# Kernel tuning notes

Measured on AMD Instinct MI355X. Metric: run time of the kernel, lower is better.

The kernel has to match this reference:

```python
import jax, jax.numpy as jnp
import numpy as np

EPS = 1e-6
DIAG_SIZE = 128  # triu band half-width (init kwarg diag_size)
NEG_INF = -1e9


def feature_map(x):
    # tanh feature map: phi(x) = tanh(x) + 1 (positive feature map)
    return jnp.tanh(x) + 1.0


def causal_dot_product(Q, K, V):
    # Q,K: [N,L,H,E], V: [N,L,H,D]
    # running KV state: S_l = sum_{s<=l} K_s V_s^T, materialized via cumsum
    kv = jnp.cumsum(jnp.einsum('nlhe,nlhd->nlhed', K, V), axis=1)  # [N,L,H,E,D]
    return jnp.einsum('nlhe,nlhed->nlhd', Q, kv)


def setup_inputs() -> dict:
    key = jax.random.key(0)
    k1, k2, k3 = jax.random.split(key, 3)
    N, L, H, E = 2, 2048, 8, 64
    queries = jax.random.normal(k1, (N, L, H, E), dtype=jnp.float32)
    keys = jax.random.normal(k2, (N, L, H, E), dtype=jnp.float32)
    values = jax.random.normal(k3, (N, L, H, E), dtype=jnp.float32)
    key_lengths_mask = jnp.ones((N, L), dtype=jnp.float32)  # all keys valid
    blend = jnp.full((1,), 0.9, dtype=jnp.float32)  # learned blend param (init 0.9)
    return {"queries": queries, "keys": keys, "values": values,
            "key_lengths_mask": key_lengths_mask, "blend": blend}


def reference(queries, keys, values, key_lengths_mask, blend):
    N, L, H, E = queries.shape
    # ---- linear attention path (kernel_1 = tanh, kernel_2 = 'none') ----
    Q1 = feature_map(queries)
    K1 = feature_map(keys) * key_lengths_mask[:, :, None, None]
    Z1 = 1.0 / (jnp.einsum('nlhi,nlhi->nlh', Q1, jnp.cumsum(K1, axis=1)) + EPS)
    LV = causal_dot_product(Q1, K1, values) * Z1[..., None]  # [N,L,H,D]
    # ---- full softmax attention path (banded by triu) ----
    softmax_temp = 1.0 / np.sqrt(E).astype(np.float32)
    QK = jnp.einsum('nlhe,nshe->nhls', queries, keys)  # [N,H,L,L]
    l_idx = jnp.arange(L)[:, None]
    s_idx = jnp.arange(L)[None, :]
    causal_add = jnp.where(s_idx <= l_idx, 0.0, NEG_INF)  # lower-triangular mask
    key_add = jnp.where(key_lengths_mask > 0, 0.0, NEG_INF)  # [N,L]
    logits = softmax_temp * (QK + causal_add[None, None] + key_add[:, None, None, :])
    A = jax.nn.softmax(logits, axis=-1)
    # torch.triu(A, diagonal=-diag_size): keep s >= l - diag_size
    band = s_idx >= (l_idx - DIAG_SIZE)
    A = jnp.where(band[None, None], A, 0.0)
    # dropout: eval mode (identity)
    SV = jnp.einsum('nhls,nshd->nlhd', A, values)
    b = blend[0]
    return b * SV + (1.0 - b) * LV
```

## Files before the change

kernel.cpp:

```cpp
#include <hip/hip_runtime.h>
#include <math.h>

#define N_ 2
#define L_ 2048
#define H_ 8
#define E_ 64
#define D_ 64
#define C_ 128
#define NC (L_/C_)
#define ROWSTRIDE (H_*E_)
#define TEMP 0.125f
#define EPS_F 1e-6f
#define NEG_INF_F (-1e9f)
#define CHUNK_WS (E_*D_ + E_)
#define NCHUNKS (N_*H_*NC)
#define TPAD 136
#define PPAD 72

typedef __attribute__((ext_vector_type(8))) short short8;
typedef __attribute__((ext_vector_type(4))) float f32x4;

__device__ __forceinline__ short f2bf(float x) {
  unsigned u = __float_as_uint(x);
  u += 0x7fffu + ((u >> 16) & 1u);
  return (short)(u >> 16);
}
__device__ __forceinline__ float bf2f(short s) {
  return __uint_as_float(((unsigned)(unsigned short)s) << 16);
}
__device__ __forceinline__ float tanh1f(float x) {
  float e = __expf(-2.f * x);
  return 2.f * __builtin_amdgcn_rcpf(1.f + e);
}

__device__ __forceinline__ void load_bf16_tile(short* __restrict__ dst,
                                               const float* __restrict__ src) {
  const int t = threadIdx.x;
#pragma unroll
  for (int it = 0; it < 4; ++it) {
    int gi = it * 256 + t;
    int row = gi >> 3, g = gi & 7;
    const float* p = src + row * ROWSTRIDE + g * 8;
    float4 a = *(const float4*)p;
    float4 b = *(const float4*)(p + 4);
    short8 v;
    v[0] = f2bf(a.x); v[1] = f2bf(a.y); v[2] = f2bf(a.z); v[3] = f2bf(a.w);
    v[4] = f2bf(b.x); v[5] = f2bf(b.y); v[6] = f2bf(b.z); v[7] = f2bf(b.w);
    int sg = g ^ (row & 7);
    *(short8*)(dst + row * 64 + sg * 8) = v;
  }
}

__device__ __forceinline__ short8 frag_ld(const short* __restrict__ buf,
                                          int rowbase, int hf, int lane) {
  int r = rowbase + (lane & 15);
  int g = (hf * 4 + (lane >> 4)) ^ (r & 7);
  return *(const short8*)(buf + r * 64 + g * 8);
}
__device__ __forceinline__ short8 frag_ldT(const short* __restrict__ buf,
                                           int nbase, int g, int lane) {
  int r = nbase + (lane & 15);
  return *(const short8*)(buf + r * TPAD + g * 8);
}
__device__ __forceinline__ short8 frag_ldP(const short* __restrict__ buf,
                                           int rowbase, int ks, int lane) {
  int r = rowbase + (lane & 15);
  int g = ks * 4 + (lane >> 4);
  return *(const short8*)(buf + r * PPAD + g * 8);
}

extern "C" __global__ void __launch_bounds__(256, 4)
k_pre(const float* __restrict__ Q, const float* __restrict__ K,
      const float* __restrict__ V, const float* __restrict__ mask,
      float* __restrict__ ws, float* __restrict__ part) {
  __shared__ short ldsA[64 * TPAD];
  __shared__ short ldsB[64 * TPAD];
  __shared__ float fmsk[C_];
  const int orig = blockIdx.x;
  const int swz = (orig & 7) * 304 + (orig >> 3);
  const int t = threadIdx.x;
  const int w = t >> 6, lane = t & 63;
  const int col_lo = lane & 15;

  if (swz < 2176) {
    const int nh = swz / 136;
    const int p = swz - nh * 136;
    int qb = (int)((sqrtf(8.f * p + 1.f) - 1.f) * 0.5f);
    while ((qb + 1) * (qb + 2) / 2 <= p) ++qb;
    while (qb * (qb + 1) / 2 > p) --qb;
    const int kb = p - qb * (qb + 1) / 2;
    const int h = nh & (H_ - 1), n = nh >> 3;

    load_bf16_tile(ldsA, Q + ((n * L_ + qb * C_) * H_ + h) * E_);
    load_bf16_tile(ldsB, K + ((n * L_ + kb * C_) * H_ + h) * E_);
    if (t < C_) fmsk[t] = mask[n * L_ + kb * C_ + t];
    __syncthreads();

    const int rowbase = w * 32;
    short8 afr[2][2];
#pragma unroll
    for (int m = 0; m < 2; ++m)
#pragma unroll
      for (int hh = 0; hh < 2; ++hh)
        afr[m][hh] = frag_ld(ldsA, rowbase + 16 * m, hh, lane);

    f32x4 acc[2][8];
#pragma unroll
    for (int m = 0; m < 2; ++m)
#pragma unroll
      for (int c = 0; c < 8; ++c) acc[m][c] = (f32x4){0.f, 0.f, 0.f, 0.f};

#pragma unroll
    for (int c = 0; c < 8; ++c) {
      short8 b0 = frag_ld(ldsB, 16 * c, 0, lane);
      short8 b1 = frag_ld(ldsB, 16 * c, 1, lane);
#pragma unroll
      for (int m = 0; m < 2; ++m) {
        acc[m][c] = __builtin_amdgcn_mfma_f32_16x16x32_bf16(afr[m][0], b0, acc[m][c], 0, 0, 0);
        acc[m][c] = __builtin_amdgcn_mfma_f32_16x16x32_bf16(afr[m][1], b1, acc[m][c], 0, 0, 0);
      }
    }

    const bool diag = (kb == qb);
    float* pout = part + (size_t)(nh * NC + qb) * C_ * 16;
#pragma unroll
    for (int m = 0; m < 2; ++m) {
      const int rbase = rowbase + 16 * m + (lane >> 4) * 4;
      float rs[4] = {0.f, 0.f, 0.f, 0.f};
#pragma unroll
      for (int c = 0; c < 8; ++c) {
        const int col = 16 * c + col_lo;
        const float madd = (fmsk[col] > 0.f) ? 0.f : NEG_INF_F;
#pragma unroll
        for (int reg = 0; reg < 4; ++reg) {
          float x = acc[m][c][reg] + madd;
          if (diag && col > rbase + reg) x += NEG_INF_F;
          rs[reg] += __expf(x * TEMP);
        }
      }
#pragma unroll
      for (int off = 1; off < 16; off <<= 1) {
#pragma unroll
        for (int reg = 0; reg < 4; ++reg) rs[reg] += __shfl_xor(rs[reg], off);
      }
      if (col_lo == 0) {
#pragma unroll
        for (int reg = 0; reg < 4; ++reg) pout[(rbase + reg) * 16 + kb] = rs[reg];
      }
    }
  } else {
    const int id = swz - 2176;
    const int nh = id >> 4, c = id & 15;
    const int h = nh & (H_ - 1), n = nh >> 3;
    const int gbase = ((n * L_ + c * C_) * H_ + h) * E_;
    const int e = t & 63, sb = t >> 6;
    const int mbase = n * L_ + c * C_;
#pragma unroll
    for (int q = 0; q < 4; ++q) {
      int s0 = sb * 32 + q * 8;
      short8 kk, vv;
#pragma unroll
      for (int j = 0; j < 8; ++j) {
        float kx = K[gbase + (s0 + j) * ROWSTRIDE + e];
        kk[j] = f2bf(tanh1f(kx) * mask[mbase + s0 + j]);
        vv[j] = f2bf(V[gbase + (s0 + j) * ROWSTRIDE + e]);
      }
      *(short8*)(ldsA + e * TPAD + (s0 >> 3) * 8) = kk;
      *(short8*)(ldsB + e * TPAD + (s0 >> 3) * 8) = vv;
    }
    __syncthreads();

    f32x4 acc[4];
#pragma unroll
    for (int nn = 0; nn < 4; ++nn) acc[nn] = (f32x4){0.f, 0.f, 0.f, 0.f};
#pragma unroll
    for (int ks = 0; ks < 4; ++ks) {
      short8 a = frag_ldT(ldsB, 16 * w, ks * 4 + (lane >> 4), lane);
#pragma unroll
      for (int nn = 0; nn < 4; ++nn) {
        short8 b = frag_ldT(ldsA, 16 * nn, ks * 4 + (lane >> 4), lane);
        acc[nn] = __builtin_amdgcn_mfma_f32_16x16x32_bf16(a, b, acc[nn], 0, 0, 0);
      }
    }
    float* wsc = ws + (size_t)(nh * NC + c) * CHUNK_WS;
    const int drow = 16 * w + ((lane >> 4) << 2);
#pragma unroll
    for (int nn = 0; nn < 4; ++nn)
#pragma unroll
      for (int reg = 0; reg < 4; ++reg)
        wsc[(16 * nn + col_lo) * D_ + drow + reg] = acc[nn][reg];
    if (t < 64) {
      float s = 0.f;
#pragma unroll
      for (int g = 0; g < 16; ++g) {
        short8 v = *(const short8*)(ldsA + t * TPAD + g * 8);
#pragma unroll
        for (int j = 0; j < 8; ++j) s += bf2f(v[j]);
      }
      wsc[E_ * D_ + t] = s;
    }
  }
}

extern "C" __global__ void __launch_bounds__(256)
k_scan(float* __restrict__ ws) {
  const int bid = blockIdx.x;
  const int swz = (bid & 7) * 34 + (bid >> 3);
  const int nh = swz / 17, seg = swz - nh * 17;
  const int idx = seg * 256 + threadIdx.x;
  if (idx >= CHUNK_WS) return;
  float* base = ws + (size_t)nh * NC * CHUNK_WS + idx;
  float v[NC];
#pragma unroll
  for (int c = 0; c < NC; ++c) v[c] = base[(size_t)c * CHUNK_WS];
  float acc = 0.f;
#pragma unroll
  for (int c = 0; c < NC; ++c) {
    base[(size_t)c * CHUNK_WS] = acc;
    acc += v[c];
  }
}

extern "C" __global__ void __launch_bounds__(256, 3)
k_fused(const float* __restrict__ Q, const float* __restrict__ K,
        const float* __restrict__ V, const float* __restrict__ mask,
        const float* __restrict__ blend, const float* __restrict__ ws,
        const float* __restrict__ part, float* __restrict__ out) {
  __shared__ short kbuf[C_ * 64];
  __shared__ short kv[64 * TPAD];
  __shared__ short pbuf[64 * PPAD];
  __shared__ float zlds[64];
  __shared__ float dinv[64];
  __shared__ float ksum[E_];
  __shared__ float kmskC[C_];
  __shared__ float kmskP[C_];

  const int orig = blockIdx.x;
  const int swz = (orig & 7) * 64 + (orig >> 3);
  const int rh = swz & 1, qb = (swz >> 1) & (NC - 1), nh = swz >> 5;
  const int h = nh & (H_ - 1), n = nh >> 3;
  const int t = threadIdx.x;
  const int w = t >> 6, lane = t & 63;
  const int rowbase = w * 16;
  const int col_lo = lane & 15;
  const int rb = rowbase + ((lane >> 4) << 2);
  const int rtile0 = rh * 64 + rb;
  const int qgbase = ((n * L_ + qb * C_ + rh * 64) * H_ + h) * E_;
  const int kbase_chunk = ((n * L_ + qb * C_) * H_ + h) * E_;
  const float* wsc = ws + (size_t)(nh * NC + qb) * CHUNK_WS;
  const float bl = blend[0];
  const float ob = 1.f - bl;
  const int d = t & 63, sb = t >> 6;
  const bool haveprev = (qb > 0);
  const int kgp = ((n * L_ + (qb - 1) * C_) * H_ + h) * E_;

  float4 qraw[2][2];
  {
    const float* qp = Q + qgbase + (rowbase + (lane & 15)) * ROWSTRIDE;
#pragma unroll
    for (int kh = 0; kh < 2; ++kh) {
      int c0 = (kh * 4 + (lane >> 4)) * 8;
      qraw[kh][0] = *(const float4*)(qp + c0);
      qraw[kh][1] = *(const float4*)(qp + c0 + 4);
    }
  }
  short8 kraw[4];
  {
    const float* mrow = mask + n * L_ + qb * C_;
#pragma unroll
    for (int it = 0; it < 4; ++it) {
      int gi = it * 256 + t, row = gi >> 3, g = gi & 7;
      const float* p = K + kbase_chunk + row * ROWSTRIDE + g * 8;
      float4 a = *(const float4*)p, b = *(const float4*)(p + 4);
      float km = mrow[row];
      float xs[8] = {a.x, a.y, a.z, a.w, b.x, b.y, b.z, b.w};
      short8 vr, v1;
#pragma unroll
      for (int j = 0; j < 8; ++j) { vr[j] = f2bf(xs[j]); v1[j] = f2bf(tanh1f(xs[j]) * km); }
      kraw[it] = vr;
      *(short8*)(kbuf + row * 64 + (g ^ (row & 7)) * 8) = v1;
    }
  }
  {
    int eb = t >> 6;
#pragma unroll
    for (int q = 0; q < 2; ++q) {
      int e0 = eb * 16 + q * 8;
      short8 v;
#pragma unroll
      for (int j = 0; j < 8; ++j) v[j] = f2bf(wsc[(e0 + j) * D_ + d]);
      *(short8*)(kv + d * TPAD + (e0 >> 3) * 8) = v;
    }
  }
  short8 vcur[4];
#pragma unroll
  for (int q = 0; q < 4; ++q) {
#pragma unroll
    for (int j = 0; j < 8; ++j)
      vcur[q][j] = f2bf(V[kbase_chunk + (sb * 32 + q * 8 + j) * ROWSTRIDE + d]);
  }
  if (t < 64) {
    ksum[t] = wsc[E_ * D_ + t];
    const float* pb = part + ((size_t)(nh * NC + qb) * C_ + rh * 64 + t) * 16;
    float4 a = *(const float4*)pb, b = *(const float4*)(pb + 4);
    float4 c = *(const float4*)(pb + 8), d4 = *(const float4*)(pb + 12);
    float vv[16] = {a.x, a.y, a.z, a.w, b.x, b.y, b.z, b.w,
                    c.x, c.y, c.z, c.w, d4.x, d4.y, d4.z, d4.w};
    float s = 0.f;
#pragma unroll
    for (int j = 0; j < 16; ++j) s += (j <= qb) ? vv[j] : 0.f;
    dinv[t] = 1.f / s;
  }
  if (t < C_) {
    kmskC[t] = mask[n * L_ + qb * C_ + t];
    kmskP[t] = haveprev ? mask[n * L_ + (qb - 1) * C_ + t] : 1.f;
  }
  __syncthreads();

  short8 af1[2], afs[2];
#pragma unroll
  for (int kh = 0; kh < 2; ++kh) {
    float xs[8] = {qraw[kh][0].x, qraw[kh][0].y, qraw[kh][0].z, qraw[kh][0].w,
                   qraw[kh][1].x, qraw[kh][1].y, qraw[kh][1].z, qraw[kh][1].w};
#pragma unroll
    for (int j = 0; j < 8; ++j) { afs[kh][j] = f2bf(xs[j]); af1[kh][j] = f2bf(tanh1f(xs[j])); }
  }
  f32x4 c1[8];
#pragma unroll
  for (int ct = 0; ct < 8; ++ct) c1[ct] = (f32x4){0.f, 0.f, 0.f, 0.f};
#pragma unroll
  for (int ct = 0; ct < 8; ++ct) {
    short8 b0 = frag_ld(kbuf, 16 * ct, 0, lane);
    short8 b1 = frag_ld(kbuf, 16 * ct, 1, lane);
    c1[ct] = __builtin_amdgcn_mfma_f32_16x16x32_bf16(af1[0], b0, c1[ct], 0, 0, 0);
    c1[ct] = __builtin_amdgcn_mfma_f32_16x16x32_bf16(af1[1], b1, c1[ct], 0, 0, 0);
  }
  {
    float zz = 0.f;
#pragma unroll
    for (int kh = 0; kh < 2; ++kh) {
      int cb = (kh * 4 + (lane >> 4)) * 8;
#pragma unroll
      for (int j = 0; j < 8; ++j) zz += bf2f(af1[kh][j]) * ksum[cb + j];
    }
    zz += __shfl_xor(zz, 16);
    zz += __shfl_xor(zz, 32);
    if (lane < 16) zlds[rowbase + lane] = zz;
  }
  float rs[4] = {0.f, 0.f, 0.f, 0.f};
#pragma unroll
  for (int ct = 0; ct < 8; ++ct) {
    int col = 16 * ct + col_lo;
#pragma unroll
    for (int reg = 0; reg < 4; ++reg) {
      if (col <= rtile0 + reg) rs[reg] += c1[ct][reg];
      else c1[ct][reg] = 0.f;
    }
  }
#pragma unroll
  for (int off = 1; off < 16; off <<= 1)
#pragma unroll
    for (int reg = 0; reg < 4; ++reg) rs[reg] += __shfl_xor(rs[reg], off);

  f32x4 accL[4];
#pragma unroll
  for (int nn = 0; nn < 4; ++nn) accL[nn] = (f32x4){0.f, 0.f, 0.f, 0.f};
#pragma unroll
  for (int ks = 0; ks < 2; ++ks) {
    short8 bf[4];
#pragma unroll
    for (int nn = 0; nn < 4; ++nn)
      bf[nn] = frag_ldT(kv, 16 * nn, ks * 4 + (lane >> 4), lane);
#pragma unroll
    for (int nn = 0; nn < 4; ++nn)
      accL[nn] = __builtin_amdgcn_mfma_f32_16x16x32_bf16(af1[ks], bf[nn], accL[nn], 0, 0, 0);
  }
  __syncthreads();

#pragma unroll
  for (int it = 0; it < 4; ++it) {
    int gi = it * 256 + t, row = gi >> 3, g = gi & 7;
    *(short8*)(kbuf + row * 64 + (g ^ (row & 7)) * 8) = kraw[it];
  }
#pragma unroll
  for (int q = 0; q < 4; ++q)
    *(short8*)(kv + d * TPAD + ((sb * 32 + q * 8) >> 3) * 8) = vcur[q];
  __syncthreads();

  short8 pk[4], pv[4];
  if (haveprev) {
#pragma unroll
    for (int it = 0; it < 4; ++it) {
      int gi = it * 256 + t, row = gi >> 3, g = gi & 7;
      const float* p = K + kgp + row * ROWSTRIDE + g * 8;
      float4 a = *(const float4*)p, b = *(const float4*)(p + 4);
      float xs[8] = {a.x, a.y, a.z, a.w, b.x, b.y, b.z, b.w};
#pragma unroll
      for (int j = 0; j < 8; ++j) pk[it][j] = f2bf(xs[j]);
    }
#pragma unroll
    for (int q = 0; q < 4; ++q)
#pragma unroll
      for (int j = 0; j < 8; ++j)
        pv[q][j] = f2bf(V[kgp + (sb * 32 + q * 8 + j) * ROWSTRIDE + d]);
  }
#pragma unroll
  for (int hh = 0; hh < 2; ++hh) {
#pragma unroll
    for (int ch = 0; ch < 4; ++ch) {
      int ct = 4 * hh + ch, colh = 16 * ch + col_lo;
#pragma unroll
      for (int reg = 0; reg < 4; ++reg)
        pbuf[(rb + reg) * PPAD + colh] = f2bf(c1[ct][reg]);
    }
#pragma unroll
    for (int ks = 0; ks < 2; ++ks) {
      short8 ap = frag_ldP(pbuf, rowbase, ks, lane);
      short8 bv[4];
#pragma unroll
      for (int nn = 0; nn < 4; ++nn)
        bv[nn] = frag_ldT(kv, 16 * nn, 8 * hh + ks * 4 + (lane >> 4), lane);
#pragma unroll
      for (int nn = 0; nn < 4; ++nn)
        accL[nn] = __builtin_amdgcn_mfma_f32_16x16x32_bf16(ap, bv[nn], accL[nn], 0, 0, 0);
    }
  }
  f32x4 accS[4];
#pragma unroll
  for (int nn = 0; nn < 4; ++nn) accS[nn] = (f32x4){0.f, 0.f, 0.f, 0.f};
  {
    f32x4 cs[8];
#pragma unroll
    for (int ct = 0; ct < 8; ++ct) cs[ct] = (f32x4){0.f, 0.f, 0.f, 0.f};
#pragma unroll
    for (int ct = 0; ct < 8; ++ct) {
      short8 b0 = frag_ld(kbuf, 16 * ct, 0, lane);
      short8 b1 = frag_ld(kbuf, 16 * ct, 1, lane);
      cs[ct] = __builtin_amdgcn_mfma_f32_16x16x32_bf16(afs[0], b0, cs[ct], 0, 0, 0);
      cs[ct] = __builtin_amdgcn_mfma_f32_16x16x32_bf16(afs[1], b1, cs[ct], 0, 0, 0);
    }
#pragma unroll
    for (int ct = 0; ct < 8; ++ct) {
      int col = 16 * ct + col_lo;
      float madd = (kmskC[col] > 0.f) ? 0.f : NEG_INF_F;
#pragma unroll
      for (int reg = 0; reg < 4; ++reg) {
        float x = cs[ct][reg] + madd;
        if (col > rtile0 + reg) x += NEG_INF_F;
        cs[ct][reg] = __expf(x * TEMP);
      }
    }
#pragma unroll
    for (int hh = 0; hh < 2; ++hh) {
#pragma unroll
      for (int ch = 0; ch < 4; ++ch) {
        int ct = 4 * hh + ch, colh = 16 * ch + col_lo;
#pragma unroll
        for (int reg = 0; reg < 4; ++reg)
          pbuf[(rb + reg) * PPAD + colh] = f2bf(cs[ct][reg]);
      }
#pragma unroll
      for (int ks = 0; ks < 2; ++ks) {
        short8 ap = frag_ldP(pbuf, rowbase, ks, lane);
        short8 bv[4];
#pragma unroll
        for (int nn = 0; nn < 4; ++nn)
          bv[nn] = frag_ldT(kv, 16 * nn, 8 * hh + ks * 4 + (lane >> 4), lane);
#pragma unroll
        for (int nn = 0; nn < 4; ++nn)
          accS[nn] = __builtin_amdgcn_mfma_f32_16x16x32_bf16(ap, bv[nn], accS[nn], 0, 0, 0);
      }
    }
  }

  if (haveprev) {
    __syncthreads();
#pragma unroll
    for (int it = 0; it < 4; ++it) {
      int gi = it * 256 + t, row = gi >> 3, g = gi & 7;
      *(short8*)(kbuf + row * 64 + (g ^ (row & 7)) * 8) = pk[it];
    }
#pragma unroll
    for (int q = 0; q < 4; ++q)
      *(short8*)(kv + d * TPAD + ((sb * 32 + q * 8) >> 3) * 8) = pv[q];
    __syncthreads();

    f32x4 cs[8];
#pragma unroll
    for (int ct = 0; ct < 8; ++ct) cs[ct] = (f32x4){0.f, 0.f, 0.f, 0.f};
#pragma unroll
    for (int ct = 0; ct < 8; ++ct) {
      short8 b0 = frag_ld(kbuf, 16 * ct, 0, lane);
      short8 b1 = frag_ld(kbuf, 16 * ct, 1, lane);
      cs[ct] = __builtin_amdgcn_mfma_f32_16x16x32_bf16(afs[0], b0, cs[ct], 0, 0, 0);
      cs[ct] = __builtin_amdgcn_mfma_f32_16x16x32_bf16(afs[1], b1, cs[ct], 0, 0, 0);
    }
#pragma unroll
    for (int ct = 0; ct < 8; ++ct) {
      int col = 16 * ct + col_lo;
      float madd = (kmskP[col] > 0.f) ? 0.f : NEG_INF_F;
#pragma unroll
      for (int reg = 0; reg < 4; ++reg) {
        float x = cs[ct][reg] + madd;
        float pp = __expf(x * TEMP);
        if (col < rtile0 + reg) pp = 0.f;
        cs[ct][reg] = pp;
      }
    }
#pragma unroll
    for (int hh = 0; hh < 2; ++hh) {
#pragma unroll
      for (int ch = 0; ch < 4; ++ch) {
        int ct = 4 * hh + ch, colh = 16 * ch + col_lo;
#pragma unroll
        for (int reg = 0; reg < 4; ++reg)
          pbuf[(rb + reg) * PPAD + colh] = f2bf(cs[ct][reg]);
      }
#pragma unroll
      for (int ks = 0; ks < 2; ++ks) {
        short8 ap = frag_ldP(pbuf, rowbase, ks, lane);
        short8 bv[4];
#pragma unroll
        for (int nn = 0; nn < 4; ++nn)
          bv[nn] = frag_ldT(kv, 16 * nn, 8 * hh + ks * 4 + (lane >> 4), lane);
#pragma unroll
        for (int nn = 0; nn < 4; ++nn)
          accS[nn] = __builtin_amdgcn_mfma_f32_16x16x32_bf16(ap, bv[nn], accS[nn], 0, 0, 0);
      }
    }
  }

  float zrf[4], sdv[4];
#pragma unroll
  for (int reg = 0; reg < 4; ++reg) {
    zrf[reg] = ob / (zlds[rb + reg] + rs[reg] + EPS_F);
    sdv[reg] = bl * dinv[rb + reg];
  }
#pragma unroll
  for (int nn = 0; nn < 4; ++nn)
#pragma unroll
    for (int reg = 0; reg < 4; ++reg)
      out[qgbase + (rb + reg) * ROWSTRIDE + 16 * nn + col_lo] =
          zrf[reg] * accL[nn][reg] + sdv[reg] * accS[nn][reg];
}

extern "C" void kernel_launch(void* const* d_in, const int* in_sizes, int n_in,
                              void* d_out, int out_size, void* d_ws, size_t ws_size,
                              hipStream_t stream) {
  (void)in_sizes; (void)n_in; (void)out_size; (void)ws_size;
  const float* Q = (const float*)d_in[0];
  const float* K = (const float*)d_in[1];
  const float* V = (const float*)d_in[2];
  const float* mask = (const float*)d_in[3];
  const float* blend = (const float*)d_in[4];
  float* out = (float*)d_out;
  float* ws = (float*)d_ws;
  float* part = ws + (size_t)NCHUNKS * CHUNK_WS;

  k_pre<<<dim3(2432), dim3(256), 0, stream>>>(Q, K, V, mask, ws, part);
  k_scan<<<dim3(272), dim3(256), 0, stream>>>(ws);
  k_fused<<<dim3(N_ * H_ * NC * 2), dim3(256), 0, stream>>>(Q, K, V, mask, blend, ws, part, out);
}
```

Measured before the change: 52.86 us.

## Move banded softmax P·V and intra-chunk linear attention into the pre-pass kernel

New measurement: 55.90 us. +5.7%, slower.

```diff
diff --git a/kernel.cpp b/kernel.cpp
--- a/kernel.cpp
+++ b/kernel.cpp
@@ -33,8 +33,9 @@
   return 2.f * __builtin_amdgcn_rcpf(1.f + e);
 }
 
-__device__ __forceinline__ void load_bf16_tile(short* __restrict__ dst,
-                                               const float* __restrict__ src) {
+template <typename F>
+__device__ __forceinline__ void stage_tile(short* __restrict__ dst,
+                                           const float* __restrict__ src, F f) {
   const int t = threadIdx.x;
 #pragma unroll
   for (int it = 0; it < 4; ++it) {
@@ -43,11 +44,25 @@
     const float* p = src + row * ROWSTRIDE + g * 8;
     float4 a = *(const float4*)p;
     float4 b = *(const float4*)(p + 4);
+    float xs[8] = {a.x, a.y, a.z, a.w, b.x, b.y, b.z, b.w};
     short8 v;
-    v[0] = f2bf(a.x); v[1] = f2bf(a.y); v[2] = f2bf(a.z); v[3] = f2bf(a.w);
-    v[4] = f2bf(b.x); v[5] = f2bf(b.y); v[6] = f2bf(b.z); v[7] = f2bf(b.w);
-    int sg = g ^ (row & 7);
-    *(short8*)(dst + row * 64 + sg * 8) = v;
+#pragma unroll
+    for (int j = 0; j < 8; ++j) v[j] = f2bf(f(xs[j], row));
+    *(short8*)(dst + row * 64 + (g ^ (row & 7)) * 8) = v;
+  }
+}
+
+__device__ __forceinline__ void stage_vT(short* __restrict__ vt,
+                                         const float* __restrict__ Vbase) {
+  const int t = threadIdx.x;
+  const int d = t & 63, sb = t >> 6;
+#pragma unroll
+  for (int q = 0; q < 4; ++q) {
+    int s0 = sb * 32 + q * 8;
+    short8 v;
+#pragma unroll
+    for (int j = 0; j < 8; ++j) v[j] = f2bf(Vbase[(s0 + j) * ROWSTRIDE + d]);
+    *(short8*)(vt + d * TPAD + (s0 >> 3) * 8) = v;
   }
 }
 
@@ -69,15 +84,69 @@
   return *(const short8*)(buf + r * PPAD + g * 8);
 }
 
-extern "C" __global__ void __launch_bounds__(256, 4)
+__device__ __forceinline__ void pv_and_store(f32x4 acc[2][8], short* __restrict__ vt,
+                                             short* __restrict__ pb,
+                                             float* __restrict__ outp,
+                                             int w, int lane, bool prevband) {
+  const int col_lo = lane & 15;
+  f32x4 accPV[2][4];
+#pragma unroll
+  for (int m = 0; m < 2; ++m)
+#pragma unroll
+    for (int nn = 0; nn < 4; ++nn) accPV[m][nn] = (f32x4){0.f, 0.f, 0.f, 0.f};
+#pragma unroll
+  for (int hh = 0; hh < 2; ++hh) {
+#pragma unroll
+    for (int m = 0; m < 2; ++m) {
+      const int rbase = 32 * w + 16 * m + ((lane >> 4) << 2);
+#pragma unroll
+      for (int ch = 0; ch < 4; ++ch) {
+        int ct = 4 * hh + ch, col = 16 * ct + col_lo;
+#pragma unroll
+        for (int reg = 0; reg < 4; ++reg) {
+          float pp = acc[m][ct][reg];
+          if (prevband && col < rbase + reg) pp = 0.f;
+          pb[(rbase + reg) * PPAD + 16 * ch + col_lo] = f2bf(pp);
+        }
+      }
+    }
+#pragma unroll
+    for (int ks = 0; ks < 2; ++ks) {
+      short8 ap[2];
+#pragma unroll
+      for (int m = 0; m < 2; ++m) ap[m] = frag_ldP(pb, 32 * w + 16 * m, ks, lane);
+      short8 bv[4];
+#pragma unroll
+      for (int nn = 0; nn < 4; ++nn)
+        bv[nn] = frag_ldT(vt, 16 * nn, 8 * hh + ks * 4 + (lane >> 4), lane);
+#pragma unroll
+      for (int m = 0; m < 2; ++m)
+#pragma unroll
+        for (int nn = 0; nn < 4; ++nn)
+          accPV[m][nn] = __builtin_amdgcn_mfma_f32_16x16x32_bf16(ap[m], bv[nn], accPV[m][nn], 0, 0, 0);
+    }
+  }
+#pragma unroll
+  for (int m = 0; m < 2; ++m) {
+    const int rbase = 32 * w + 16 * m + ((lane >> 4) << 2);
+#pragma unroll
+    for (int nn = 0; nn < 4; ++nn)
+#pragma unroll
+      for (int reg = 0; reg < 4; ++reg)
+        outp[(rbase + reg) * D_ + 16 * nn + col_lo] = accPV[m][nn][reg];
+  }
+}
+
+extern "C" __global__ void __launch_bounds__(256, 3)
 k_pre(const float* __restrict__ Q, const float* __restrict__ K,
       const float* __restrict__ V, const float* __restrict__ mask,
-      float* __restrict__ ws, float* __restrict__ part) {
-  __shared__ short ldsA[64 * TPAD];
-  __shared__ short ldsB[64 * TPAD];
+      float* __restrict__ ws, float* __restrict__ part,
+      float* __restrict__ pvd, float* __restrict__ pvp,
+      float* __restrict__ lvl, float* __restrict__ rsuml) {
+  __shared__ short lds[17920];
   __shared__ float fmsk[C_];
   const int orig = blockIdx.x;
-  const int swz = (orig & 7) * 304 + (orig >> 3);
+  const int swz = (orig & 7) * 336 + (orig >> 3);
   const int t = threadIdx.x;
   const int w = t >> 6, lane = t & 63;
   const int col_lo = lane & 15;
@@ -90,9 +159,11 @@
     while (qb * (qb + 1) / 2 > p) --qb;
     const int kb = p - qb * (qb + 1) / 2;
     const int h = nh & (H_ - 1), n = nh >> 3;
-
-    load_bf16_tile(ldsA, Q + ((n * L_ + qb * C_) * H_ + h) * E_);
-    load_bf16_tile(ldsB, K + ((n * L_ + kb * C_) * H_ + h) * E_);
+    const int koff = ((n * L_ + kb * C_) * H_ + h) * E_;
+
+    stage_tile(lds, Q + ((n * L_ + qb * C_) * H_ + h) * E_,
+               [](float x, int) { return x; });
+    stage_tile(lds + 8192, K + koff, [](float x, int) { return x; });
     if (t < C_) fmsk[t] = mask[n * L_ + kb * C_ + t];
     __syncthreads();
 
@@ -102,18 +173,17 @@
     for (int m = 0; m < 2; ++m)
 #pragma unroll
       for (int hh = 0; hh < 2; ++hh)
-        afr[m][hh] = frag_ld(ldsA, rowbase + 16 * m, hh, lane);
+        afr[m][hh] = frag_ld(lds, rowbase + 16 * m, hh, lane);
 
     f32x4 acc[2][8];
 #pragma unroll
     for (int m = 0; m < 2; ++m)
 #pragma unroll
       for (int c = 0; c < 8; ++c) acc[m][c] = (f32x4){0.f, 0.f, 0.f, 0.f};
-
 #pragma unroll
     for (int c = 0; c < 8; ++c) {
-      short8 b0 = frag_ld(ldsB, 16 * c, 0, lane);
-      short8 b1 = frag_ld(ldsB, 16 * c, 1, lane);
+      short8 b0 = frag_ld(lds + 8192, 16 * c, 0, lane);
+      short8 b1 = frag_ld(lds + 8192, 16 * c, 1, lane);
 #pragma unroll
       for (int m = 0; m < 2; ++m) {
         acc[m][c] = __builtin_amdgcn_mfma_f32_16x16x32_bf16(afr[m][0], b0, acc[m][c], 0, 0, 0);
@@ -121,11 +191,11 @@
       }
     }
 
-    const bool diag = (kb == qb);
+    const bool diag = (kb == qb), prev = (kb == qb - 1);
     float* pout = part + (size_t)(nh * NC + qb) * C_ * 16;
 #pragma unroll
     for (int m = 0; m < 2; ++m) {
-      const int rbase = rowbase + 16 * m + (lane >> 4) * 4;
+      const int rbase = rowbase + 16 * m + ((lane >> 4) << 2);
       float rs[4] = {0.f, 0.f, 0.f, 0.f};
 #pragma unroll
       for (int c = 0; c < 8; ++c) {
@@ -135,7 +205,9 @@
         for (int reg = 0; reg < 4; ++reg) {
           float x = acc[m][c][reg] + madd;
           if (diag && col > rbase + reg) x += NEG_INF_F;
-          rs[reg] += __expf(x * TEMP);
+          float e = __expf(x * TEMP);
+          acc[m][c][reg] = e;
+          rs[reg] += e;
         }
       }
 #pragma unroll
@@ -148,13 +220,23 @@
         for (int reg = 0; reg < 4; ++reg) pout[(rbase + reg) * 16 + kb] = rs[reg];
       }
     }
-  } else {
+
+    if (diag || prev) {
+      __syncthreads();
+      stage_vT(lds, V + koff);
+      __syncthreads();
+      float* outp = (diag ? pvd : pvp) + (size_t)(nh * NC + qb) * (C_ * D_);
+      pv_and_store(acc, lds, lds + 8704, outp, w, lane, prev);
+    }
+  } else if (swz < 2432) {
     const int id = swz - 2176;
     const int nh = id >> 4, c = id & 15;
     const int h = nh & (H_ - 1), n = nh >> 3;
     const int gbase = ((n * L_ + c * C_) * H_ + h) * E_;
     const int e = t & 63, sb = t >> 6;
     const int mbase = n * L_ + c * C_;
+    short* k1T = lds;
+    short* vT2 = lds + 8704;
 #pragma unroll
     for (int q = 0; q < 4; ++q) {
       int s0 = sb * 32 + q * 8;
@@ -165,8 +247,8 @@
         kk[j] = f2bf(tanh1f(kx) * mask[mbase + s0 + j]);
         vv[j] = f2bf(V[gbase + (s0 + j) * ROWSTRIDE + e]);
       }
-      *(short8*)(ldsA + e * TPAD + (s0 >> 3) * 8) = kk;
-      *(short8*)(ldsB + e * TPAD + (s0 >> 3) * 8) = vv;
+      *(short8*)(k1T + e * TPAD + (s0 >> 3) * 8) = kk;
+      *(short8*)(vT2 + e * TPAD + (s0 >> 3) * 8) = vv;
     }
     __syncthreads();
 
@@ -175,10 +257,10 @@
     for (int nn = 0; nn < 4; ++nn) acc[nn] = (f32x4){0.f, 0.f, 0.f, 0.f};
 #pragma unroll
     for (int ks = 0; ks < 4; ++ks) {
-      short8 a = frag_ldT(ldsB, 16 * w, ks * 4 + (lane >> 4), lane);
+      short8 a = frag_ldT(vT2, 16 * w, ks * 4 + (lane >> 4), lane);
 #pragma unroll
       for (int nn = 0; nn < 4; ++nn) {
-        short8 b = frag_ldT(ldsA, 16 * nn, ks * 4 + (lane >> 4), lane);
+        short8 b = frag_ldT(k1T, 16 * nn, ks * 4 + (lane >> 4), lane);
         acc[nn] = __builtin_amdgcn_mfma_f32_16x16x32_bf16(a, b, acc[nn], 0, 0, 0);
       }
     }
@@ -193,12 +275,76 @@
       float s = 0.f;
 #pragma unroll
       for (int g = 0; g < 16; ++g) {
-        short8 v = *(const short8*)(ldsA + t * TPAD + g * 8);
+        short8 v = *(const short8*)(k1T + t * TPAD + g * 8);
 #pragma unroll
         for (int j = 0; j < 8; ++j) s += bf2f(v[j]);
       }
       wsc[E_ * D_ + t] = s;
     }
+  } else {
+    const int id = swz - 2432;
+    const int nh = id >> 4, qb = id & 15;
+    const int h = nh & (H_ - 1), n = nh >> 3;
+    const int gbase = ((n * L_ + qb * C_) * H_ + h) * E_;
+    const float* mrow = mask + n * L_ + qb * C_;
+
+    stage_tile(lds, Q + gbase, [](float x, int) { return tanh1f(x); });
+    stage_tile(lds + 8192, K + gbase,
+               [mrow](float x, int row) { return tanh1f(x) * mrow[row]; });
+    __syncthreads();
+
+    const int rowbase = w * 32;
+    short8 afr[2][2];
+#pragma unroll
+    for (int m = 0; m < 2; ++m)
+#pragma unroll
+      for (int hh = 0; hh < 2; ++hh)
+        afr[m][hh] = frag_ld(lds, rowbase + 16 * m, hh, lane);
+
+    f32x4 acc[2][8];
+#pragma unroll
+    for (int m = 0; m < 2; ++m)
+#pragma unroll
+      for (int c = 0; c < 8; ++c) acc[m][c] = (f32x4){0.f, 0.f, 0.f, 0.f};
+#pragma unroll
+    for (int c = 0; c < 8; ++c) {
+      short8 b0 = frag_ld(lds + 8192, 16 * c, 0, lane);
+      short8 b1 = frag_ld(lds + 8192, 16 * c, 1, lane);
+#pragma unroll
+      for (int m = 0; m < 2; ++m) {
+        acc[m][c] = __builtin_amdgcn_mfma_f32_16x16x32_bf16(afr[m][0], b0, acc[m][c], 0, 0, 0);
+        acc[m][c] = __builtin_amdgcn_mfma_f32_16x16x32_bf16(afr[m][1], b1, acc[m][c], 0, 0, 0);
+      }
+    }
+    float* rout = rsuml + (size_t)(nh * NC + qb) * C_;
+#pragma unroll
+    for (int m = 0; m < 2; ++m) {
+      const int rbase = rowbase + 16 * m + ((lane >> 4) << 2);
+      float rs[4] = {0.f, 0.f, 0.f, 0.f};
+#pragma unroll
+      for (int c = 0; c < 8; ++c) {
+        const int col = 16 * c + col_lo;
+#pragma unroll
+        for (int reg = 0; reg < 4; ++reg) {
+          if (col <= rbase + reg) rs[reg] += acc[m][c][reg];
+          else acc[m][c][reg] = 0.f;
+        }
+      }
+#pragma unroll
+      for (int off = 1; off < 16; off <<= 1) {
+#pragma unroll
+        for (int reg = 0; reg < 4; ++reg) rs[reg] += __shfl_xor(rs[reg], off);
+      }
+      if (col_lo == 0) {
+#pragma unroll
+        for (int reg = 0; reg < 4; ++reg) rout[rbase + reg] = rs[reg];
+      }
+    }
+    __syncthreads();
+    stage_vT(lds, V + gbase);
+    __syncthreads();
+    pv_and_store(acc, lds, lds + 8704,
+                 lvl + (size_t)(nh * NC + qb) * (C_ * D_), w, lane, false);
   }
 }
 
@@ -221,19 +367,16 @@
   }
 }
 
-extern "C" __global__ void __launch_bounds__(256, 3)
-k_fused(const float* __restrict__ Q, const float* __restrict__ K,
-        const float* __restrict__ V, const float* __restrict__ mask,
-        const float* __restrict__ blend, const float* __restrict__ ws,
-        const float* __restrict__ part, float* __restrict__ out) {
-  __shared__ short kbuf[C_ * 64];
+extern "C" __global__ void __launch_bounds__(256)
+k_fused(const float* __restrict__ Q, const float* __restrict__ blend,
+        const float* __restrict__ ws, const float* __restrict__ part,
+        const float* __restrict__ pvd, const float* __restrict__ pvp,
+        const float* __restrict__ lvl, const float* __restrict__ rsuml,
+        float* __restrict__ out) {
   __shared__ short kv[64 * TPAD];
-  __shared__ short pbuf[64 * PPAD];
   __shared__ float zlds[64];
   __shared__ float dinv[64];
   __shared__ float ksum[E_];
-  __shared__ float kmskC[C_];
-  __shared__ float kmskP[C_];
 
   const int orig = blockIdx.x;
   const int swz = (orig & 7) * 64 + (orig >> 3);
@@ -246,39 +389,23 @@
   const int rb = rowbase + ((lane >> 4) << 2);
   const int rtile0 = rh * 64 + rb;
   const int qgbase = ((n * L_ + qb * C_ + rh * 64) * H_ + h) * E_;
-  const int kbase_chunk = ((n * L_ + qb * C_) * H_ + h) * E_;
   const float* wsc = ws + (size_t)(nh * NC + qb) * CHUNK_WS;
   const float bl = blend[0];
   const float ob = 1.f - bl;
-  const int d = t & 63, sb = t >> 6;
-  const bool haveprev = (qb > 0);
-  const int kgp = ((n * L_ + (qb - 1) * C_) * H_ + h) * E_;
-
-  float4 qraw[2][2];
+  const int d = t & 63;
+  const size_t tb = (size_t)(nh * NC + qb) * (C_ * D_);
+
+  short8 af1[2];
   {
     const float* qp = Q + qgbase + (rowbase + (lane & 15)) * ROWSTRIDE;
 #pragma unroll
     for (int kh = 0; kh < 2; ++kh) {
       int c0 = (kh * 4 + (lane >> 4)) * 8;
-      qraw[kh][0] = *(const float4*)(qp + c0);
-      qraw[kh][1] = *(const float4*)(qp + c0 + 4);
-    }
-  }
-  short8 kraw[4];
-  {
-    const float* mrow = mask + n * L_ + qb * C_;
-#pragma unroll
-    for (int it = 0; it < 4; ++it) {
-      int gi = it * 256 + t, row = gi >> 3, g = gi & 7;
-      const float* p = K + kbase_chunk + row * ROWSTRIDE + g * 8;
-      float4 a = *(const float4*)p, b = *(const float4*)(p + 4);
-      float km = mrow[row];
+      float4 a = *(const float4*)(qp + c0);
+      float4 b = *(const float4*)(qp + c0 + 4);
       float xs[8] = {a.x, a.y, a.z, a.w, b.x, b.y, b.z, b.w};
-      short8 vr, v1;
-#pragma unroll
-      for (int j = 0; j < 8; ++j) { vr[j] = f2bf(xs[j]); v1[j] = f2bf(tanh1f(xs[j]) * km); }
-      kraw[it] = vr;
-      *(short8*)(kbuf + row * 64 + (g ^ (row & 7)) * 8) = v1;
+#pragma unroll
+      for (int j = 0; j < 8; ++j) af1[kh][j] = f2bf(tanh1f(xs[j]));
     }
   }
   {
@@ -291,13 +418,6 @@
       for (int j = 0; j < 8; ++j) v[j] = f2bf(wsc[(e0 + j) * D_ + d]);
       *(short8*)(kv + d * TPAD + (e0 >> 3) * 8) = v;
     }
-  }
-  short8 vcur[4];
-#pragma unroll
-  for (int q = 0; q < 4; ++q) {
-#pragma unroll
-    for (int j = 0; j < 8; ++j)
-      vcur[q][j] = f2bf(V[kbase_chunk + (sb * 32 + q * 8 + j) * ROWSTRIDE + d]);
   }
   if (t < 64) {
     ksum[t] = wsc[E_ * D_ + t];
@@ -311,30 +431,22 @@
     for (int j = 0; j < 16; ++j) s += (j <= qb) ? vv[j] : 0.f;
     dinv[t] = 1.f / s;
   }
-  if (t < C_) {
-    kmskC[t] = mask[n * L_ + qb * C_ + t];
-    kmskP[t] = haveprev ? mask[n * L_ + (qb - 1) * C_ + t] : 1.f;
-  }
+  float rsv[4];
+#pragma unroll
+  for (int reg = 0; reg < 4; ++reg)
+    rsv[reg] = rsuml[(size_t)(nh * NC + qb) * C_ + rtile0 + reg];
+  float lvv[4][4], pvv[4][4];
+#pragma unroll
+  for (int nn = 0; nn < 4; ++nn)
+#pragma unroll
+    for (int reg = 0; reg < 4; ++reg) {
+      size_t a = tb + (size_t)(rtile0 + reg) * D_ + 16 * nn + col_lo;
+      lvv[nn][reg] = lvl[a];
+      float pd = pvd[a];
+      pvv[nn][reg] = (qb > 0) ? pd + pvp[a] : pd;
+    }
   __syncthreads();
 
-  short8 af1[2], afs[2];
-#pragma unroll
-  for (int kh = 0; kh < 2; ++kh) {
-    float xs[8] = {qraw[kh][0].x, qraw[kh][0].y, qraw[kh][0].z, qraw[kh][0].w,
-                   qraw[kh][1].x, qraw[kh][1].y, qraw[kh][1].z, qraw[kh][1].w};
-#pragma unroll
-    for (int j = 0; j < 8; ++j) { afs[kh][j] = f2bf(xs[j]); af1[kh][j] = f2bf(tanh1f(xs[j])); }
-  }
-  f32x4 c1[8];
-#pragma unroll
-  for (int ct = 0; ct < 8; ++ct) c1[ct] = (f32x4){0.f, 0.f, 0.f, 0.f};
-#pragma unroll
-  for (int ct = 0; ct < 8; ++ct) {
-    short8 b0 = frag_ld(kbuf, 16 * ct, 0, lane);
-    short8 b1 = frag_ld(kbuf, 16 * ct, 1, lane);
-    c1[ct] = __builtin_amdgcn_mfma_f32_16x16x32_bf16(af1[0], b0, c1[ct], 0, 0, 0);
-    c1[ct] = __builtin_amdgcn_mfma_f32_16x16x32_bf16(af1[1], b1, c1[ct], 0, 0, 0);
-  }
   {
     float zz = 0.f;
 #pragma unroll
@@ -347,21 +459,6 @@
     zz += __shfl_xor(zz, 32);
     if (lane < 16) zlds[rowbase + lane] = zz;
   }
-  float rs[4] = {0.f, 0.f, 0.f, 0.f};
-#pragma unroll
-  for (int ct = 0; ct < 8; ++ct) {
-    int col = 16 * ct + col_lo;
-#pragma unroll
-    for (int reg = 0; reg < 4; ++reg) {
-      if (col <= rtile0 + reg) rs[reg] += c1[ct][reg];
-      else c1[ct][reg] = 0.f;
-    }
-  }
-#pragma unroll
-  for (int off = 1; off < 16; off <<= 1)
-#pragma unroll
-    for (int reg = 0; reg < 4; ++reg) rs[reg] += __shfl_xor(rs[reg], off);
-
   f32x4 accL[4];
 #pragma unroll
   for (int nn = 0; nn < 4; ++nn) accL[nn] = (f32x4){0.f, 0.f, 0.f, 0.f};
@@ -375,165 +472,11 @@
     for (int nn = 0; nn < 4; ++nn)
       accL[nn] = __builtin_amdgcn_mfma_f32_16x16x32_bf16(af1[ks], bf[nn], accL[nn], 0, 0, 0);
   }
-  __syncthreads();
-
-#pragma unroll
-  for (int it = 0; it < 4; ++it) {
-    int gi = it * 256 + t, row = gi >> 3, g = gi & 7;
-    *(short8*)(kbuf + row * 64 + (g ^ (row & 7)) * 8) = kraw[it];
-  }
-#pragma unroll
-  for (int q = 0; q < 4; ++q)
-    *(short8*)(kv + d * TPAD + ((sb * 32 + q * 8) >> 3) * 8) = vcur[q];
-  __syncthreads();
-
-  short8 pk[4], pv[4];
-  if (haveprev) {
-#pragma unroll
-    for (int it = 0; it < 4; ++it) {
-      int gi = it * 256 + t, row = gi >> 3, g = gi & 7;
-      const float* p = K + kgp + row * ROWSTRIDE + g * 8;
-      float4 a = *(const float4*)p, b = *(const float4*)(p + 4);
-      float xs[8] = {a.x, a.y, a.z, a.w, b.x, b.y, b.z, b.w};
-#pragma unroll
-      for (int j = 0; j < 8; ++j) pk[it][j] = f2bf(xs[j]);
-    }
-#pragma unroll
-    for (int q = 0; q < 4; ++q)
-#pragma unroll
-      for (int j = 0; j < 8; ++j)
-        pv[q][j] = f2bf(V[kgp + (sb * 32 + q * 8 + j) * ROWSTRIDE + d]);
-  }
-#pragma unroll
-  for (int hh = 0; hh < 2; ++hh) {
-#pragma unroll
-    for (int ch = 0; ch < 4; ++ch) {
-      int ct = 4 * hh + ch, colh = 16 * ch + col_lo;
-#pragma unroll
-      for (int reg = 0; reg < 4; ++reg)
-        pbuf[(rb + reg) * PPAD + colh] = f2bf(c1[ct][reg]);
-    }
-#pragma unroll
-    for (int ks = 0; ks < 2; ++ks) {
-      short8 ap = frag_ldP(pbuf, rowbase, ks, lane);
-      short8 bv[4];
-#pragma unroll
-      for (int nn = 0; nn < 4; ++nn)
-        bv[nn] = frag_ldT(kv, 16 * nn, 8 * hh + ks * 4 + (lane >> 4), lane);
-#pragma unroll
-      for (int nn = 0; nn < 4; ++nn)
-        accL[nn] = __builtin_amdgcn_mfma_f32_16x16x32_bf16(ap, bv[nn], accL[nn], 0, 0, 0);
-    }
-  }
-  f32x4 accS[4];
-#pragma unroll
-  for (int nn = 0; nn < 4; ++nn) accS[nn] = (f32x4){0.f, 0.f, 0.f, 0.f};
-  {
-    f32x4 cs[8];
-#pragma unroll
-    for (int ct = 0; ct < 8; ++ct) cs[ct] = (f32x4){0.f, 0.f, 0.f, 0.f};
-#pragma unroll
-    for (int ct = 0; ct < 8; ++ct) {
-      short8 b0 = frag_ld(kbuf, 16 * ct, 0, lane);
-      short8 b1 = frag_ld(kbuf, 16 * ct, 1, lane);
-      cs[ct] = __builtin_amdgcn_mfma_f32_16x16x32_bf16(afs[0], b0, cs[ct], 0, 0, 0);
-      cs[ct] = __builtin_amdgcn_mfma_f32_16x16x32_bf16(afs[1], b1, cs[ct], 0, 0, 0);
-    }
-#pragma unroll
-    for (int ct = 0; ct < 8; ++ct) {
-      int col = 16 * ct + col_lo;
-      float madd = (kmskC[col] > 0.f) ? 0.f : NEG_INF_F;
-#pragma unroll
-      for (int reg = 0; reg < 4; ++reg) {
-        float x = cs[ct][reg] + madd;
-        if (col > rtile0 + reg) x += NEG_INF_F;
-        cs[ct][reg] = __expf(x * TEMP);
-      }
-    }
-#pragma unroll
-    for (int hh = 0; hh < 2; ++hh) {
-#pragma unroll
-      for (int ch = 0; ch < 4; ++ch) {
-        int ct = 4 * hh + ch, colh = 16 * ch + col_lo;
-#pragma unroll
-        for (int reg = 0; reg < 4; ++reg)
-          pbuf[(rb + reg) * PPAD + colh] = f2bf(cs[ct][reg]);
-      }
-#pragma unroll
-      for (int ks = 0; ks < 2; ++ks) {
-        short8 ap = frag_ldP(pbuf, rowbase, ks, lane);
-        short8 bv[4];
-#pragma unroll
-        for (int nn = 0; nn < 4; ++nn)
-          bv[nn] = frag_ldT(kv, 16 * nn, 8 * hh + ks * 4 + (lane >> 4), lane);
-#pragma unroll
-        for (int nn = 0; nn < 4; ++nn)
-          accS[nn] = __builtin_amdgcn_mfma_f32_16x16x32_bf16(ap, bv[nn], accS[nn], 0, 0, 0);
-      }
-    }
-  }
-
-  if (haveprev) {
-    __syncthreads();
-#pragma unroll
-    for (int it = 0; it < 4; ++it) {
-      int gi = it * 256 + t, row = gi >> 3, g = gi & 7;
-      *(short8*)(kbuf + row * 64 + (g ^ (row & 7)) * 8) = pk[it];
-    }
-#pragma unroll
-    for (int q = 0; q < 4; ++q)
-      *(short8*)(kv + d * TPAD + ((sb * 32 + q * 8) >> 3) * 8) = pv[q];
-    __syncthreads();
-
-    f32x4 cs[8];
-#pragma unroll
-    for (int ct = 0; ct < 8; ++ct) cs[ct] = (f32x4){0.f, 0.f, 0.f, 0.f};
-#pragma unroll
-    for (int ct = 0; ct < 8; ++ct) {
-      short8 b0 = frag_ld(kbuf, 16 * ct, 0, lane);
-      short8 b1 = frag_ld(kbuf, 16 * ct, 1, lane);
-      cs[ct] = __builtin_amdgcn_mfma_f32_16x16x32_bf16(afs[0], b0, cs[ct], 0, 0, 0);
-      cs[ct] = __builtin_amdgcn_mfma_f32_16x16x32_bf16(afs[1], b1, cs[ct], 0, 0, 0);
-    }
-#pragma unroll
-    for (int ct = 0; ct < 8; ++ct) {
-      int col = 16 * ct + col_lo;
-      float madd = (kmskP[col] > 0.f) ? 0.f : NEG_INF_F;
-#pragma unroll
-      for (int reg = 0; reg < 4; ++reg) {
-        float x = cs[ct][reg] + madd;
-        float pp = __expf(x * TEMP);
-        if (col < rtile0 + reg) pp = 0.f;
-        cs[ct][reg] = pp;
-      }
-    }
-#pragma unroll
-    for (int hh = 0; hh < 2; ++hh) {
-#pragma unroll
-      for (int ch = 0; ch < 4; ++ch) {
-        int ct = 4 * hh + ch, colh = 16 * ch + col_lo;
-#pragma unroll
-        for (int reg = 0; reg < 4; ++reg)
-          pbuf[(rb + reg) * PPAD + colh] = f2bf(cs[ct][reg]);
-      }
-#pragma unroll
-      for (int ks = 0; ks < 2; ++ks) {
-        short8 ap = frag_ldP(pbuf, rowbase, ks, lane);
-        short8 bv[4];
-#pragma unroll
-        for (int nn = 0; nn < 4; ++nn)
-          bv[nn] = frag_ldT(kv, 16 * nn, 8 * hh + ks * 4 + (lane >> 4), lane);
-#pragma unroll
-        for (int nn = 0; nn < 4; ++nn)
-          accS[nn] = __builtin_amdgcn_mfma_f32_16x16x32_bf16(ap, bv[nn], accS[nn], 0, 0, 0);
-      }
-    }
-  }
 
   float zrf[4], sdv[4];
 #pragma unroll
   for (int reg = 0; reg < 4; ++reg) {
-    zrf[reg] = ob / (zlds[rb + reg] + rs[reg] + EPS_F);
+    zrf[reg] = ob / (zlds[rb + reg] + rsv[reg] + EPS_F);
     sdv[reg] = bl * dinv[rb + reg];
   }
 #pragma unroll
@@ -541,7 +484,7 @@
 #pragma unroll
     for (int reg = 0; reg < 4; ++reg)
       out[qgbase + (rb + reg) * ROWSTRIDE + 16 * nn + col_lo] =
-          zrf[reg] * accL[nn][reg] + sdv[reg] * accS[nn][reg];
+          zrf[reg] * (accL[nn][reg] + lvv[nn][reg]) + sdv[reg] * pvv[nn][reg];
 }
 
 extern "C" void kernel_launch(void* const* d_in, const int* in_sizes, int n_in,
@@ -555,9 +498,13 @@
   const float* blend = (const float*)d_in[4];
   float* out = (float*)d_out;
   float* ws = (float*)d_ws;
-  float* part = ws + (size_t)NCHUNKS * CHUNK_WS;
-
-  k_pre<<<dim3(2432), dim3(256), 0, stream>>>(Q, K, V, mask, ws, part);
+  float* part  = ws + (size_t)NCHUNKS * CHUNK_WS;
+  float* pvd   = part + (size_t)NCHUNKS * C_ * 16;
+  float* pvp   = pvd + (size_t)NCHUNKS * C_ * D_;
+  float* lvl   = pvp + (size_t)NCHUNKS * C_ * D_;
+  float* rsuml = lvl + (size_t)NCHUNKS * C_ * D_;
+
+  k_pre<<<dim3(2688), dim3(256), 0, stream>>>(Q, K, V, mask, ws, part, pvd, pvp, lvl, rsuml);
   k_scan<<<dim3(272), dim3(256), 0, stream>>>(ws);
-  k_fused<<<dim3(N_ * H_ * NC * 2), dim3(256), 0, stream>>>(Q, K, V, mask, blend, ws, part, out);
-}
+  k_fused<<<dim3(N_ * H_ * NC * 2), dim3(256), 0, stream>>>(Q, blend, ws, part, pvd, pvp, lvl, rsuml, out);
+}
```
